# Kernel optimization log

Measured on AMD Instinct MI355X. Metric: run time of the kernel, lower is better.

## Reference

```python
import jax, jax.numpy as jnp
import numpy as np

N_NODES = 500_000
N_EDGES = 1_000_000
IN_DIM = 128
HID_DIM = 256
BN_EPS = 1e-5


def setup_inputs() -> dict:
    key = jax.random.key(0)
    ks = jax.random.split(key, 4)
    out = jax.random.normal(ks[0], (N_NODES, IN_DIM), dtype=jnp.float32)
    edge_label_index = jax.random.randint(ks[1], (2, N_EDGES), 0, N_NODES, dtype=jnp.int64)
    # Kaiming-uniform-ish init scale for linears
    W1 = jax.random.normal(ks[2], (IN_DIM, HID_DIM), dtype=jnp.float32) * (1.0 / np.sqrt(IN_DIM))
    b1 = jnp.zeros((HID_DIM,), dtype=jnp.float32)
    gamma = jnp.ones((HID_DIM,), dtype=jnp.float32)
    beta = jnp.zeros((HID_DIM,), dtype=jnp.float32)
    W2 = jax.random.normal(ks[3], (HID_DIM, 1), dtype=jnp.float32) * (1.0 / np.sqrt(HID_DIM))
    b2 = jnp.zeros((1,), dtype=jnp.float32)
    return {"out": out, "edge_label_index": edge_label_index,
            "W1": W1, "b1": b1, "gamma": gamma, "beta": beta, "W2": W2, "b2": b2}


def reference(out, edge_label_index, W1, b1, gamma, beta, W2, b2):
    src = edge_label_index[0]
    dst = edge_label_index[1]
    dot = out[src] * out[dst]                      # [E, IN_DIM] gather + hadamard
    h = dot @ W1 + b1                              # [E, HID_DIM]
    # BatchNorm1d (training mode: batch statistics, biased variance)
    mean = jnp.mean(h, axis=0)
    var = jnp.mean(jnp.square(h - mean), axis=0)
    h = (h - mean) * jax.lax.rsqrt(var + BN_EPS) * gamma + beta
    h = jax.nn.relu(h)
    y = h @ W2 + b2                                # [E, 1]
    return y.reshape(-1)
```

## Files before the change

### kernel.cpp

```cpp
#include <hip/hip_runtime.h>
#include <hip/hip_bf16.h>

#define E_EDGES   1000000
#define TILE_E    64
#define N_TILES   (E_EDGES / TILE_E)
#define IN_DIM_K  128
#define HID_N     256
#define BN_EPS_F  1e-5f
#define MAIN_GRID 256

typedef __attribute__((ext_vector_type(4))) float f32x4;
typedef __attribute__((ext_vector_type(8))) short bf16x8;

__device__ __forceinline__ unsigned short f2bf(float f) {
    __hip_bfloat16 h = __float2bfloat16(f);
    return *reinterpret_cast<unsigned short*>(&h);
}
__device__ __forceinline__ unsigned pack2(float lo, float hi) {
    return (unsigned)f2bf(lo) | ((unsigned)f2bf(hi) << 16);
}

union FragU { uint4 u; bf16x8 v; unsigned w[4]; };

__global__ void zero_stats_kernel(float* g) {
    g[threadIdx.x] = 0.0f;
}

__global__ void finalize_stats_kernel(const float* __restrict__ gstat,
                                      const float* __restrict__ gamma,
                                      const float* __restrict__ beta,
                                      float* __restrict__ nAB) {
    int c = threadIdx.x;
    float inv_e = 1.0f / (float)E_EDGES;
    float mean = gstat[c] * inv_e;
    float var  = fmaxf(gstat[256 + c] * inv_e - mean * mean, 0.0f);
    float a = gamma[c] * rsqrtf(var + BN_EPS_F);
    nAB[c] = a;
    nAB[256 + c] = beta[c] - mean * a;
}

template <bool STATS>
__global__ __launch_bounds__(512, 2)
void hadamard_mlp_kernel(const float* __restrict__ nodes,
                         const int* __restrict__ eidx,
                         const float* __restrict__ W1,
                         const float* __restrict__ W2,
                         const float* __restrict__ b2p,
                         float* __restrict__ gstat,
                         const float* __restrict__ nAB,
                         float* __restrict__ y)
{
    __shared__ unsigned sh_d[2][TILE_E * 68];
    __shared__ float s_red[2][256];

    const int tid  = threadIdx.x;
    const int lane = tid & 63;
    const int w    = tid >> 6;
    const int wm   = w >> 2;
    const int wn   = w & 3;
    const int l15  = lane & 15;
    const int l4   = lane >> 4;

    bf16x8 bfrag[4][4];
    #pragma unroll
    for (int nt = 0; nt < 4; ++nt) {
        const int c = wn * 64 + nt * 16 + l15;
        #pragma unroll
        for (int kk = 0; kk < 4; ++kk) {
            const int kb = kk * 32 + 8 * l4;
            FragU t;
            #pragma unroll
            for (int j = 0; j < 4; ++j) {
                float w0 = W1[(kb + 2 * j    ) * HID_N + c];
                float w1 = W1[(kb + 2 * j + 1) * HID_N + c];
                t.w[j] = pack2(w0, w1);
            }
            bfrag[nt][kk] = t.v;
        }
    }

    float a_n[4], b_n[4], w2_n[4];
    if (!STATS) {
        #pragma unroll
        for (int nt = 0; nt < 4; ++nt) {
            const int c = wn * 64 + nt * 16 + l15;
            a_n[nt]  = nAB[c];
            b_n[nt]  = nAB[256 + c];
            w2_n[nt] = W2[c];
        }
    }
    const float b2v = b2p[0];

    float s1[4] = {0.f, 0.f, 0.f, 0.f};
    float s2[4] = {0.f, 0.f, 0.f, 0.f};

    const int ge   = tid >> 3;
    const int part = tid & 7;

    float4 g[8];
    int si, di;

    const int t0 = blockIdx.x;
    {
        const int e0 = t0 * TILE_E + ge;
        si = eidx[e0];
        di = eidx[E_EDGES + e0];
    }
    {
        const float4* ps = reinterpret_cast<const float4*>(nodes + (size_t)si * IN_DIM_K) + part * 4;
        const float4* pd = reinterpret_cast<const float4*>(nodes + (size_t)di * IN_DIM_K) + part * 4;
        #pragma unroll
        for (int j = 0; j < 4; ++j) { g[j] = ps[j]; g[4 + j] = pd[j]; }
    }
    {
        const int t1 = t0 + gridDim.x;
        if (t1 < N_TILES) {
            const int e1 = t1 * TILE_E + ge;
            si = eidx[e1];
            di = eidx[E_EDGES + e1];
        }
    }

    int cur = 0;
    int ptile = -1;

    for (int tile = t0; tile < N_TILES; tile += gridDim.x) {
        {
            unsigned buf[8];
            #pragma unroll
            for (int j = 0; j < 4; ++j) {
                buf[2 * j]     = pack2(g[j].x * g[4 + j].x, g[j].y * g[4 + j].y);
                buf[2 * j + 1] = pack2(g[j].z * g[4 + j].z, g[j].w * g[4 + j].w);
            }
            unsigned* dst = sh_d[cur] + ge * 68 + part * 8;
            *reinterpret_cast<uint4*>(dst)     = *reinterpret_cast<const uint4*>(buf);
            *reinterpret_cast<uint4*>(dst + 4) = *reinterpret_cast<const uint4*>(buf + 4);
        }
        const int ntile = tile + gridDim.x;
        if (ntile < N_TILES) {
            const float4* ps = reinterpret_cast<const float4*>(nodes + (size_t)si * IN_DIM_K) + part * 4;
            const float4* pd = reinterpret_cast<const float4*>(nodes + (size_t)di * IN_DIM_K) + part * 4;
            #pragma unroll
            for (int j = 0; j < 4; ++j) { g[j] = ps[j]; g[4 + j] = pd[j]; }
        }
        {
            const int n2 = tile + 2 * gridDim.x;
            if (n2 < N_TILES) {
                const int e2 = n2 * TILE_E + ge;
                si = eidx[e2];
                di = eidx[E_EDGES + e2];
            }
        }

        __syncthreads();

        if (!STATS && ptile >= 0 && tid < TILE_E) {
            const float* r = s_red[cur ^ 1];
            y[ptile * TILE_E + tid] = r[tid] + r[64 + tid] + r[128 + tid]
                                    + r[192 + tid] + b2v;
        }

        f32x4 acc[2][4] = {};
        #pragma unroll
        for (int kk = 0; kk < 4; ++kk) {
            bf16x8 af[2];
            #pragma unroll
            for (int mt = 0; mt < 2; ++mt) {
                const int row = wm * 32 + mt * 16 + l15;
                FragU t;
                t.u = *reinterpret_cast<const uint4*>(sh_d[cur] + row * 68 + kk * 16 + 4 * l4);
                af[mt] = t.v;
            }
            #pragma unroll
            for (int mt = 0; mt < 2; ++mt)
                #pragma unroll
                for (int nt = 0; nt < 4; ++nt)
                    acc[mt][nt] = __builtin_amdgcn_mfma_f32_16x16x32_bf16(
                        af[mt], bfrag[nt][kk], acc[mt][nt], 0, 0, 0);
        }

        if (STATS) {
            #pragma unroll
            for (int nt = 0; nt < 4; ++nt) {
                float t1s = 0.f, t2s = 0.f;
                #pragma unroll
                for (int mt = 0; mt < 2; ++mt)
                    #pragma unroll
                    for (int r = 0; r < 4; ++r) {
                        float v = acc[mt][nt][r];
                        t1s += v;
                        t2s += v * v;
                    }
                s1[nt] += t1s;
                s2[nt] += t2s;
            }
        } else {
            float pw[2][4];
            #pragma unroll
            for (int mt = 0; mt < 2; ++mt)
                #pragma unroll
                for (int r = 0; r < 4; ++r) {
                    float acc_y = 0.f;
                    #pragma unroll
                    for (int nt = 0; nt < 4; ++nt) {
                        float z = acc[mt][nt][r] * a_n[nt] + b_n[nt];
                        z = fmaxf(z, 0.f);
                        acc_y += z * w2_n[nt];
                    }
                    pw[mt][r] = acc_y;
                }
            #pragma unroll
            for (int off = 1; off < 16; off <<= 1)
                #pragma unroll
                for (int mt = 0; mt < 2; ++mt)
                    #pragma unroll
                    for (int r = 0; r < 4; ++r)
                        pw[mt][r] += __shfl_xor(pw[mt][r], off, 64);
            if (l15 == 0) {
                #pragma unroll
                for (int mt = 0; mt < 2; ++mt)
                    #pragma unroll
                    for (int r = 0; r < 4; ++r) {
                        const int el = wm * 32 + mt * 16 + l4 * 4 + r;
                        s_red[cur][wn * 64 + el] = pw[mt][r];
                    }
            }
            ptile = tile;
        }
        cur ^= 1;
    }

    if (STATS) {
        #pragma unroll
        for (int nt = 0; nt < 4; ++nt) {
            s1[nt] += __shfl_xor(s1[nt], 16, 64);
            s1[nt] += __shfl_xor(s1[nt], 32, 64);
            s2[nt] += __shfl_xor(s2[nt], 16, 64);
            s2[nt] += __shfl_xor(s2[nt], 32, 64);
        }
        if (l4 == 0) {
            #pragma unroll
            for (int nt = 0; nt < 4; ++nt) {
                const int c = wn * 64 + nt * 16 + l15;
                atomicAdd(&gstat[c],       s1[nt]);
                atomicAdd(&gstat[256 + c], s2[nt]);
            }
        }
    } else {
        __syncthreads();
        if (ptile >= 0 && tid < TILE_E) {
            const float* r = s_red[cur ^ 1];
            y[ptile * TILE_E + tid] = r[tid] + r[64 + tid] + r[128 + tid]
                                    + r[192 + tid] + b2v;
        }
    }
}

extern "C" void kernel_launch(void* const* d_in, const int* in_sizes, int n_in,
                              void* d_out, int out_size, void* d_ws, size_t ws_size,
                              hipStream_t stream) {
    const float* nodes = (const float*)d_in[0];
    const int*   eidx  = (const int*)d_in[1];
    const float* W1    = (const float*)d_in[2];
    const float* gamma = (const float*)d_in[4];
    const float* beta  = (const float*)d_in[5];
    const float* W2    = (const float*)d_in[6];
    const float* b2    = (const float*)d_in[7];

    float* ws    = (float*)d_ws;
    float* gstat = ws;
    float* nAB   = ws + 512;
    float* y     = (float*)d_out;

    zero_stats_kernel<<<1, 512, 0, stream>>>(gstat);
    hadamard_mlp_kernel<true><<<MAIN_GRID, 512, 0, stream>>>(
        nodes, eidx, W1, W2, b2, gstat, nAB, y);
    finalize_stats_kernel<<<1, 256, 0, stream>>>(gstat, gamma, beta, nAB);
    hadamard_mlp_kernel<false><<<MAIN_GRID, 512, 0, stream>>>(
        nodes, eidx, W1, W2, b2, gstat, nAB, y);
}
```

Baseline: 322.2 us.

## Pre-convert node table to bf16, shrink tiles, fuse BN finalize into main kernel

Adds a conversion pass that writes the node feature table as bf16 into the workspace, so both gather passes read half the bytes per edge and multiply in bf16-derived floats. Tiles shrink to 32 edges with 256-thread blocks and a larger grid, the BN finalize kernel is folded into the second pass's prologue, the stats zeroing is folded into the conversion kernel, and MFMA sections get raised wave priority. The cost is an extra full read and write of the node table each call, a dependence on workspace size, and slightly different rounding because the hadamard product is now formed from bf16 inputs.

```diff
diff --git a/kernel.cpp b/kernel.cpp
--- a/kernel.cpp
+++ b/kernel.cpp
@@ -1,13 +1,15 @@
 #include <hip/hip_runtime.h>
 #include <hip/hip_bf16.h>
 
+#define N_NODES   500000
 #define E_EDGES   1000000
-#define TILE_E    64
+#define TILE_E    32
 #define N_TILES   (E_EDGES / TILE_E)
 #define IN_DIM_K  128
 #define HID_N     256
 #define BN_EPS_F  1e-5f
-#define MAIN_GRID 256
+#define MAIN_GRID 768
+#define CONV_GRID 2048
 
 typedef __attribute__((ext_vector_type(4))) float f32x4;
 typedef __attribute__((ext_vector_type(8))) short bf16x8;
@@ -19,6 +21,13 @@
 __device__ __forceinline__ unsigned pack2(float lo, float hi) {
     return (unsigned)f2bf(lo) | ((unsigned)f2bf(hi) << 16);
 }
+__device__ __forceinline__ unsigned bfmul2(unsigned a, unsigned b) {
+    float alo = __uint_as_float(a << 16);
+    float ahi = __uint_as_float(a & 0xffff0000u);
+    float blo = __uint_as_float(b << 16);
+    float bhi = __uint_as_float(b & 0xffff0000u);
+    return pack2(alo * blo, ahi * bhi);
+}
 
 union FragU { uint4 u; bf16x8 v; unsigned w[4]; };
 
@@ -26,38 +35,47 @@
     g[threadIdx.x] = 0.0f;
 }
 
-__global__ void finalize_stats_kernel(const float* __restrict__ gstat,
-                                      const float* __restrict__ gamma,
-                                      const float* __restrict__ beta,
-                                      float* __restrict__ nAB) {
-    int c = threadIdx.x;
-    float inv_e = 1.0f / (float)E_EDGES;
-    float mean = gstat[c] * inv_e;
-    float var  = fmaxf(gstat[256 + c] * inv_e - mean * mean, 0.0f);
-    float a = gamma[c] * rsqrtf(var + BN_EPS_F);
-    nAB[c] = a;
-    nAB[256 + c] = beta[c] - mean * a;
-}
-
-template <bool STATS>
-__global__ __launch_bounds__(512, 2)
+__global__ void convert_nodes_kernel(const float* __restrict__ in,
+                                     unsigned* __restrict__ out,
+                                     float* __restrict__ gstat) {
+    if (blockIdx.x == 0) {
+        gstat[threadIdx.x] = 0.0f;
+        gstat[256 + threadIdx.x] = 0.0f;
+    }
+    const size_t n4 = (size_t)N_NODES * IN_DIM_K / 8;
+    size_t i = (size_t)blockIdx.x * blockDim.x + threadIdx.x;
+    const size_t stride = (size_t)gridDim.x * blockDim.x;
+    for (; i < n4; i += stride) {
+        float4 a = reinterpret_cast<const float4*>(in)[2 * i];
+        float4 b = reinterpret_cast<const float4*>(in)[2 * i + 1];
+        uint4 o;
+        o.x = pack2(a.x, a.y);
+        o.y = pack2(a.z, a.w);
+        o.z = pack2(b.x, b.y);
+        o.w = pack2(b.z, b.w);
+        reinterpret_cast<uint4*>(out)[i] = o;
+    }
+}
+
+template <bool STATS, bool BFT>
+__global__ __launch_bounds__(256, 3)
 void hadamard_mlp_kernel(const float* __restrict__ nodes,
+                         const unsigned* __restrict__ nbf,
                          const int* __restrict__ eidx,
                          const float* __restrict__ W1,
                          const float* __restrict__ W2,
                          const float* __restrict__ b2p,
                          float* __restrict__ gstat,
-                         const float* __restrict__ nAB,
+                         const float* __restrict__ gamma,
+                         const float* __restrict__ beta,
                          float* __restrict__ y)
 {
     __shared__ unsigned sh_d[2][TILE_E * 68];
-    __shared__ float s_red[2][256];
+    __shared__ float s_red[2][128];
 
     const int tid  = threadIdx.x;
     const int lane = tid & 63;
-    const int w    = tid >> 6;
-    const int wm   = w >> 2;
-    const int wn   = w & 3;
+    const int wn   = tid >> 6;
     const int l15  = lane & 15;
     const int l4   = lane >> 4;
 
@@ -81,11 +99,17 @@
 
     float a_n[4], b_n[4], w2_n[4];
     if (!STATS) {
+        const float inv_e = 1.0f / (float)E_EDGES;
         #pragma unroll
         for (int nt = 0; nt < 4; ++nt) {
             const int c = wn * 64 + nt * 16 + l15;
-            a_n[nt]  = nAB[c];
-            b_n[nt]  = nAB[256 + c];
+            float s  = gstat[c];
+            float ss = gstat[256 + c];
+            float mean = s * inv_e;
+            float var  = fmaxf(ss * inv_e - mean * mean, 0.0f);
+            float a = gamma[c] * rsqrtf(var + BN_EPS_F);
+            a_n[nt]  = a;
+            b_n[nt]  = beta[c] - mean * a;
             w2_n[nt] = W2[c];
         }
     }
@@ -97,76 +121,81 @@
     const int ge   = tid >> 3;
     const int part = tid & 7;
 
-    float4 g[8];
+    uint4  g[4];
+    float4 h[8];
     int si, di;
+
+#define GATHER(SNODE, DNODE)                                                   \
+    if constexpr (BFT) {                                                       \
+        const uint4* ps = reinterpret_cast<const uint4*>(nbf + (size_t)(SNODE) * 64) + part * 2; \
+        const uint4* pd = reinterpret_cast<const uint4*>(nbf + (size_t)(DNODE) * 64) + part * 2; \
+        g[0] = ps[0]; g[1] = ps[1]; g[2] = pd[0]; g[3] = pd[1];                \
+    } else {                                                                   \
+        const float4* ps = reinterpret_cast<const float4*>(nodes + (size_t)(SNODE) * IN_DIM_K) + part * 4; \
+        const float4* pd = reinterpret_cast<const float4*>(nodes + (size_t)(DNODE) * IN_DIM_K) + part * 4; \
+        _Pragma("unroll")                                                      \
+        for (int j = 0; j < 4; ++j) { h[j] = ps[j]; h[4 + j] = pd[j]; }        \
+    }
 
     const int t0 = blockIdx.x;
     {
         const int e0 = t0 * TILE_E + ge;
-        si = eidx[e0];
-        di = eidx[E_EDGES + e0];
-    }
-    {
-        const float4* ps = reinterpret_cast<const float4*>(nodes + (size_t)si * IN_DIM_K) + part * 4;
-        const float4* pd = reinterpret_cast<const float4*>(nodes + (size_t)di * IN_DIM_K) + part * 4;
-        #pragma unroll
-        for (int j = 0; j < 4; ++j) { g[j] = ps[j]; g[4 + j] = pd[j]; }
-    }
-    {
-        const int t1 = t0 + gridDim.x;
-        if (t1 < N_TILES) {
-            const int e1 = t1 * TILE_E + ge;
-            si = eidx[e1];
-            di = eidx[E_EDGES + e1];
-        }
+        const int s = eidx[e0];
+        const int d = eidx[E_EDGES + e0];
+        GATHER(s, d);
+    }
+    si = di = 0;
+    if (t0 + MAIN_GRID < N_TILES) {
+        const int e = (t0 + MAIN_GRID) * TILE_E + ge;
+        si = eidx[e];  di = eidx[E_EDGES + e];
     }
 
     int cur = 0;
     int ptile = -1;
 
-    for (int tile = t0; tile < N_TILES; tile += gridDim.x) {
+    for (int tile = t0; tile < N_TILES; tile += MAIN_GRID) {
         {
             unsigned buf[8];
-            #pragma unroll
-            for (int j = 0; j < 4; ++j) {
-                buf[2 * j]     = pack2(g[j].x * g[4 + j].x, g[j].y * g[4 + j].y);
-                buf[2 * j + 1] = pack2(g[j].z * g[4 + j].z, g[j].w * g[4 + j].w);
+            if constexpr (BFT) {
+                buf[0] = bfmul2(g[0].x, g[2].x); buf[1] = bfmul2(g[0].y, g[2].y);
+                buf[2] = bfmul2(g[0].z, g[2].z); buf[3] = bfmul2(g[0].w, g[2].w);
+                buf[4] = bfmul2(g[1].x, g[3].x); buf[5] = bfmul2(g[1].y, g[3].y);
+                buf[6] = bfmul2(g[1].z, g[3].z); buf[7] = bfmul2(g[1].w, g[3].w);
+            } else {
+                #pragma unroll
+                for (int j = 0; j < 4; ++j) {
+                    buf[2*j]   = pack2(h[j].x * h[4+j].x, h[j].y * h[4+j].y);
+                    buf[2*j+1] = pack2(h[j].z * h[4+j].z, h[j].w * h[4+j].w);
+                }
             }
             unsigned* dst = sh_d[cur] + ge * 68 + part * 8;
             *reinterpret_cast<uint4*>(dst)     = *reinterpret_cast<const uint4*>(buf);
             *reinterpret_cast<uint4*>(dst + 4) = *reinterpret_cast<const uint4*>(buf + 4);
         }
-        const int ntile = tile + gridDim.x;
-        if (ntile < N_TILES) {
-            const float4* ps = reinterpret_cast<const float4*>(nodes + (size_t)si * IN_DIM_K) + part * 4;
-            const float4* pd = reinterpret_cast<const float4*>(nodes + (size_t)di * IN_DIM_K) + part * 4;
-            #pragma unroll
-            for (int j = 0; j < 4; ++j) { g[j] = ps[j]; g[4 + j] = pd[j]; }
-        }
-        {
-            const int n2 = tile + 2 * gridDim.x;
-            if (n2 < N_TILES) {
-                const int e2 = n2 * TILE_E + ge;
-                si = eidx[e2];
-                di = eidx[E_EDGES + e2];
-            }
+        if (tile + MAIN_GRID < N_TILES) {
+            GATHER(si, di);
+        }
+        if (tile + 2 * MAIN_GRID < N_TILES) {
+            const int e = (tile + 2 * MAIN_GRID) * TILE_E + ge;
+            si = eidx[e];  di = eidx[E_EDGES + e];
         }
 
         __syncthreads();
 
         if (!STATS && ptile >= 0 && tid < TILE_E) {
             const float* r = s_red[cur ^ 1];
-            y[ptile * TILE_E + tid] = r[tid] + r[64 + tid] + r[128 + tid]
-                                    + r[192 + tid] + b2v;
+            y[ptile * TILE_E + tid] = r[tid] + r[32 + tid] + r[64 + tid]
+                                    + r[96 + tid] + b2v;
         }
 
         f32x4 acc[2][4] = {};
+        __builtin_amdgcn_s_setprio(1);
         #pragma unroll
         for (int kk = 0; kk < 4; ++kk) {
             bf16x8 af[2];
             #pragma unroll
             for (int mt = 0; mt < 2; ++mt) {
-                const int row = wm * 32 + mt * 16 + l15;
+                const int row = mt * 16 + l15;
                 FragU t;
                 t.u = *reinterpret_cast<const uint4*>(sh_d[cur] + row * 68 + kk * 16 + 4 * l4);
                 af[mt] = t.v;
@@ -178,6 +207,7 @@
                     acc[mt][nt] = __builtin_amdgcn_mfma_f32_16x16x32_bf16(
                         af[mt], bfrag[nt][kk], acc[mt][nt], 0, 0, 0);
         }
+        __builtin_amdgcn_s_setprio(0);
 
         if (STATS) {
             #pragma unroll
@@ -221,14 +251,15 @@
                 for (int mt = 0; mt < 2; ++mt)
                     #pragma unroll
                     for (int r = 0; r < 4; ++r) {
-                        const int el = wm * 32 + mt * 16 + l4 * 4 + r;
-                        s_red[cur][wn * 64 + el] = pw[mt][r];
+                        const int el = mt * 16 + l4 * 4 + r;
+                        s_red[cur][wn * 32 + el] = pw[mt][r];
                     }
             }
             ptile = tile;
         }
         cur ^= 1;
     }
+#undef GATHER
 
     if (STATS) {
         #pragma unroll
@@ -250,8 +281,8 @@
         __syncthreads();
         if (ptile >= 0 && tid < TILE_E) {
             const float* r = s_red[cur ^ 1];
-            y[ptile * TILE_E + tid] = r[tid] + r[64 + tid] + r[128 + tid]
-                                    + r[192 + tid] + b2v;
+            y[ptile * TILE_E + tid] = r[tid] + r[32 + tid] + r[64 + tid]
+                                    + r[96 + tid] + b2v;
         }
     }
 }
@@ -269,13 +300,23 @@
 
     float* ws    = (float*)d_ws;
     float* gstat = ws;
-    float* nAB   = ws + 512;
+    unsigned* nbf = (unsigned*)((char*)d_ws + 4096);
     float* y     = (float*)d_out;
 
-    zero_stats_kernel<<<1, 512, 0, stream>>>(gstat);
-    hadamard_mlp_kernel<true><<<MAIN_GRID, 512, 0, stream>>>(
-        nodes, eidx, W1, W2, b2, gstat, nAB, y);
-    finalize_stats_kernel<<<1, 256, 0, stream>>>(gstat, gamma, beta, nAB);
-    hadamard_mlp_kernel<false><<<MAIN_GRID, 512, 0, stream>>>(
-        nodes, eidx, W1, W2, b2, gstat, nAB, y);
-}
+    const size_t T_BYTES = (size_t)N_NODES * IN_DIM_K * 2;
+    const bool fast = ws_size >= (4096 + T_BYTES);
+
+    if (fast) {
+        convert_nodes_kernel<<<CONV_GRID, 256, 0, stream>>>(nodes, nbf, gstat);
+        hadamard_mlp_kernel<true, true><<<MAIN_GRID, 256, 0, stream>>>(
+            nodes, nbf, eidx, W1, W2, b2, gstat, gamma, beta, y);
+        hadamard_mlp_kernel<false, true><<<MAIN_GRID, 256, 0, stream>>>(
+            nodes, nbf, eidx, W1, W2, b2, gstat, gamma, beta, y);
+    } else {
+        zero_stats_kernel<<<1, 512, 0, stream>>>(gstat);
+        hadamard_mlp_kernel<true, false><<<MAIN_GRID, 256, 0, stream>>>(
+            nodes, nbf, eidx, W1, W2, b2, gstat, gamma, beta, y);
+        hadamard_mlp_kernel<false, false><<<MAIN_GRID, 256, 0, stream>>>(
+            nodes, nbf, eidx, W1, W2, b2, gstat, gamma, beta, y);
+    }
+}
```

After: 259.5 us (median of 2 runs). 19.5% less time.
